# Optimization experiments

Measured on AMD Instinct MI355X. Metric: run time of the kernel, lower is better.

Reference implementation:

```python
import jax, jax.numpy as jnp
import numpy as np

B, NQ, NV = 4, 16384, 16384
DIM, FRAMES = 64, 4
D = DIM * FRAMES            # embed_dims = 256
HEADS, POINTS, LEVELS = 8, 4, 1
HD = D // HEADS             # head_dim = 32
HL, WL = 128, 128           # single-level feature map, HL*WL == NV
EPS = 1e-6


def setup_inputs() -> dict:
    key = jax.random.key(0)
    ks = jax.random.split(key, 14)
    inp = {
        "query": jax.random.normal(ks[0], (B, NQ, D), jnp.float32),
        "feat": jax.random.normal(ks[1], (B, NV, D), jnp.float32),
        "reference_points": jax.random.uniform(ks[2], (B, NQ, LEVELS, 2), jnp.float32),
        "spatial_shapes": jnp.array([[HL, WL]], jnp.int32),
        "level_start_index": jnp.array([0], jnp.int32),
        # LayerNorm params
        "qn_scale": jnp.ones((D,), jnp.float32),
        "qn_bias": jnp.zeros((D,), jnp.float32),
        "fn_scale": jnp.ones((D,), jnp.float32),
        "fn_bias": jnp.zeros((D,), jnp.float32),
        # MSDeformAttn projections
        "W_value": jax.random.normal(ks[3], (D, D), jnp.float32) / np.sqrt(D),
        "b_value": jnp.zeros((D,), jnp.float32),
        "W_off": jax.random.normal(ks[4], (D, HEADS * LEVELS * POINTS * 2), jnp.float32) * 0.01,
        "b_off": jax.random.normal(ks[5], (HEADS * LEVELS * POINTS * 2,), jnp.float32) * 0.5,
        "W_attn": jax.random.normal(ks[6], (D, HEADS * LEVELS * POINTS), jnp.float32) * 0.02,
        "b_attn": jnp.zeros((HEADS * LEVELS * POINTS,), jnp.float32),
        "W_out": jax.random.normal(ks[7], (D, D), jnp.float32) / np.sqrt(D),
        "b_out": jnp.zeros((D,), jnp.float32),
        # gamma is a learned scale (init 0 in the module; randomized here so it contributes)
        "gamma": jax.random.normal(ks[8], (D,), jnp.float32) * 0.1,
    }
    return inp


def _layer_norm(x, scale, bias):
    mu = jnp.mean(x, axis=-1, keepdims=True)
    var = jnp.mean(jnp.square(x - mu), axis=-1, keepdims=True)
    return (x - mu) * jax.lax.rsqrt(var + EPS) * scale + bias


def _bilinear_gather(v, loc, Hl, Wl):
    # v:   [B, H, N, hd] flattened level values (row-major HxW)
    # loc: [B, H, NQ, P, 2] normalized sampling locations in [0,1]
    # grid_sample semantics: align_corners=False, zero padding
    x = loc[..., 0] * Wl - 0.5
    y = loc[..., 1] * Hl - 0.5
    x0 = jnp.floor(x); y0 = jnp.floor(y)
    x1 = x0 + 1.0;     y1 = y0 + 1.0
    wx1 = x - x0; wx0 = 1.0 - wx1
    wy1 = y - y0; wy0 = 1.0 - wy1
    out = 0.0
    for xi, yi, w in ((x0, y0, wx0 * wy0), (x1, y0, wx1 * wy0),
                      (x0, y1, wx0 * wy1), (x1, y1, wx1 * wy1)):
        inb = (xi >= 0) & (xi < Wl) & (yi >= 0) & (yi < Hl)
        idx = (jnp.clip(yi, 0, Hl - 1) * Wl + jnp.clip(xi, 0, Wl - 1)).astype(jnp.int32)
        Bc, Hc, NQc, Pc = idx.shape
        g = jnp.take_along_axis(v, idx.reshape(Bc, Hc, NQc * Pc)[..., None], axis=2)
        g = g.reshape(Bc, Hc, NQc, Pc, -1)          # [B, H, NQ, P, hd]
        out = out + g * (w * inb)[..., None]
    return out


def reference(query, feat, reference_points, spatial_shapes, level_start_index,
              qn_scale, qn_bias, fn_scale, fn_bias,
              W_value, b_value, W_off, b_off, W_attn, b_attn, W_out, b_out, gamma):
    Bq, nq, _ = query.shape
    q = _layer_norm(query, qn_scale, qn_bias)
    v = _layer_norm(feat, fn_scale, fn_bias)

    # value projection -> per-head values [B, H, NV, hd]
    value = (v @ W_value + b_value).reshape(Bq, -1, HEADS, HD).transpose(0, 2, 1, 3)

    # sampling offsets [B, NQ, H, L, P, 2] and attention weights (softmax over L*P)
    off = (q @ W_off + b_off).reshape(Bq, nq, HEADS, LEVELS, POINTS, 2)
    aw = jax.nn.softmax((q @ W_attn + b_attn).reshape(Bq, nq, HEADS, LEVELS * POINTS), axis=-1)
    aw = aw.reshape(Bq, nq, HEADS, LEVELS, POINTS)

    ss = np.asarray(spatial_shapes)          # static level geometry
    lsi = np.asarray(level_start_index)
    offset_norm = ss[:, ::-1].astype(np.float32)  # (W, H) per level
    # sampling locations [B, NQ, H, L, P, 2]
    loc = reference_points[:, :, None, :, None, :] + off / offset_norm[None, None, None, :, None, :]

    acc = jnp.zeros((Bq, HEADS, nq, HD), query.dtype)
    for l in range(LEVELS):
        Hl, Wl = int(ss[l, 0]), int(ss[l, 1])
        start = int(lsi[l])
        v_l = value[:, :, start:start + Hl * Wl]                # [B, H, Hl*Wl, hd]
        loc_l = loc[:, :, :, l].transpose(0, 2, 1, 3, 4)        # [B, H, NQ, P, 2]
        sampled = _bilinear_gather(v_l, loc_l, Hl, Wl)          # [B, H, NQ, P, hd]
        aw_l = aw[:, :, :, l].transpose(0, 2, 1, 3)             # [B, H, NQ, P]
        acc = acc + jnp.einsum('bhnpd,bhnp->bhnd', sampled, aw_l)

    out = acc.transpose(0, 2, 1, 3).reshape(Bq, nq, D) @ W_out + b_out
    return query + gamma * out
```

## Files before the change

### kernel.cpp

```cpp
#include <hip/hip_runtime.h>

#define NQ 16384
#define NV 16384
#define DMODEL 256
#define SAMPN (4 * 16384 * 8)
#define VPLANE 65536

typedef __bf16 bf16x8 __attribute__((ext_vector_type(8)));
typedef float f32x4 __attribute__((ext_vector_type(4)));

__device__ __forceinline__ unsigned short f2bf(float x) {
    union { float f; unsigned int u; } v; v.f = x;
    unsigned int r = v.u + 0x7fff + ((v.u >> 16) & 1);
    return (unsigned short)(r >> 16);
}
__device__ __forceinline__ float blo(unsigned int u) {
    union { unsigned int u; float f; } v; v.u = u << 16; return v.f;
}
__device__ __forceinline__ float bhi(unsigned int u) {
    union { unsigned int u; float f; } v; v.u = u & 0xFFFF0000u; return v.f;
}
__device__ __forceinline__ f32x4 mfma16(bf16x8 a, bf16x8 b, f32x4 c) {
    return __builtin_amdgcn_mfma_f32_16x16x32_bf16(a, b, c, 0, 0, 0);
}

__global__ __launch_bounds__(256) void k_prep(
    const float* __restrict__ Wv, const float* __restrict__ Woff,
    const float* __restrict__ Wattn, const float* __restrict__ Wout,
    const float* __restrict__ fns, const float* __restrict__ fnb,
    const float* __restrict__ qns, const float* __restrict__ qnb,
    const float* __restrict__ b_value, const float* __restrict__ b_off,
    const float* __restrict__ b_attn,
    unsigned short* __restrict__ WtV, unsigned short* __restrict__ WtC,
    unsigned short* __restrict__ WtO,
    float* __restrict__ csumV, float* __restrict__ preV,
    float* __restrict__ csumC, float* __restrict__ preC) {
    const int blk = blockIdx.x;
    if (blk < 608) {
        int t = blk * 256 + threadIdx.x;
        if (t < 65536) { int n = t >> 8, k = t & 255; WtV[t] = f2bf(fns[k] * Wv[k * 256 + n]); return; }
        t -= 65536;
        if (t < 65536) { int n = t >> 8, k = t & 255; WtO[t] = f2bf(Wout[k * 256 + n]); return; }
        t -= 65536;
        if (t < 24576) {
            int j = t >> 8, k = t & 255;
            float w = (j < 64) ? Woff[k * 64 + j] : Wattn[k * 32 + (j - 64)];
            WtC[j * 256 + k] = f2bf(qns[k] * w);
        }
        return;
    }
    if (blk < 612) {
        __shared__ float sCS[4][64], sPR[4][64];
        const int nl = threadIdx.x & 63;
        const int n = (blk - 608) * 64 + nl;
        const int kp = threadIdx.x >> 6;
        float cs = 0.f, pr = 0.f;
        for (int k = kp * 64; k < kp * 64 + 64; ++k) {
            float w = Wv[k * 256 + n];
            cs += fns[k] * w;
            pr += fnb[k] * w;
        }
        sCS[kp][nl] = cs; sPR[kp][nl] = pr;
        __syncthreads();
        if (threadIdx.x < 64) {
            int nn = (blk - 608) * 64 + threadIdx.x;
            csumV[nn] = sCS[0][threadIdx.x] + sCS[1][threadIdx.x] + sCS[2][threadIdx.x] + sCS[3][threadIdx.x];
            preV[nn] = sPR[0][threadIdx.x] + sPR[1][threadIdx.x] + sPR[2][threadIdx.x] + sPR[3][threadIdx.x]
                       + b_value[nn];
        }
        return;
    }
    {
        __shared__ float sCS[2][96], sPR[2][96];
        const int t = threadIdx.x;
        if (t < 192) {
            const int n = t % 96;
            const int kp = t / 96;
            float cs = 0.f, pr = 0.f;
            for (int k = kp * 128; k < kp * 128 + 128; ++k) {
                float w = (n < 64) ? Woff[k * 64 + n] : Wattn[k * 32 + (n - 64)];
                cs += qns[k] * w;
                pr += qnb[k] * w;
            }
            sCS[kp][n] = cs; sPR[kp][n] = pr;
        }
        __syncthreads();
        if (t < 96) {
            csumC[t] = sCS[0][t] + sCS[1][t];
            preC[t] = sPR[0][t] + sPR[1][t] + ((t < 64) ? b_off[t] : b_attn[t - 64]);
        }
        return;
    }
}

#define STAGE_LNSTATS64(srcptr)                                                       \
    {                                                                                 \
        const int t = threadIdx.x;                                                    \
        const float4* src4 = (const float4*)((srcptr) + (size_t)m0 * 256);            \
        _Pragma("unroll 8") for (int i = 0; i < 16; ++i) {                            \
            float4 x = src4[i * 256 + t];                                             \
            const int row = i * 4 + (t >> 6);                                         \
            uint2 pk;                                                                 \
            pk.x = (unsigned)f2bf(x.x) | ((unsigned)f2bf(x.y) << 16);                 \
            pk.y = (unsigned)f2bf(x.z) | ((unsigned)f2bf(x.w) << 16);                 \
            *(uint2*)&A[row * 264 + (t & 63) * 4] = pk;                               \
        }                                                                             \
    }                                                                                 \
    __syncthreads();                                                                  \
    {                                                                                 \
        const int t = threadIdx.x;                                                    \
        const int r = t >> 2, h = t & 3;                                              \
        float s = 0.f, sq = 0.f;                                                      \
        _Pragma("unroll") for (int j = 0; j < 8; ++j) {                               \
            uint4 u = *(const uint4*)&A[r * 264 + h * 64 + j * 8];                    \
            float v0 = blo(u.x), v1 = bhi(u.x), v2 = blo(u.y), v3 = bhi(u.y);         \
            float v4 = blo(u.z), v5 = bhi(u.z), v6 = blo(u.w), v7 = bhi(u.w);         \
            s += v0 + v1 + v2 + v3 + v4 + v5 + v6 + v7;                               \
            sq += v0 * v0 + v1 * v1 + v2 * v2 + v3 * v3 +                             \
                  v4 * v4 + v5 * v5 + v6 * v6 + v7 * v7;                              \
        }                                                                             \
        s += __shfl_xor(s, 1);  sq += __shfl_xor(sq, 1);                              \
        s += __shfl_xor(s, 2);  sq += __shfl_xor(sq, 2);                              \
        if (h == 0) {                                                                 \
            float mu = s * 0.00390625f;                                               \
            muL[r] = mu;                                                              \
            rsL[r] = rsqrtf(sq * 0.00390625f - mu * mu + 1e-6f);                      \
        }                                                                             \
    }

#define MFMA_STEP4(bf, kk)                                                            \
    _Pragma("unroll") for (int m = 0; m < 4; ++m) {                                   \
        bf16x8 a = *(const bf16x8*)&A[(m * 16 + lrow) * 264 + (kk) * 32 + lk];        \
        _Pragma("unroll") for (int i = 0; i < 4; ++i)                                 \
            acc[i][m] = mfma16(bf[i], a, acc[i][m]);                                  \
    }

__global__ __launch_bounds__(256, 4) void k_mlp(
    const float* __restrict__ feat, const float* __restrict__ csumV,
    const float* __restrict__ preV, const unsigned short* __restrict__ WtV,
    unsigned short* __restrict__ value,
    const float* __restrict__ query, const float* __restrict__ refpt,
    const float* __restrict__ csumC, const float* __restrict__ preC,
    const unsigned short* __restrict__ WtC, float4* __restrict__ samples) {
    __shared__ unsigned short A[64 * 264];
    __shared__ float muL[64], rsL[64];
    const int blk = blockIdx.x;
    const int m0 = (blk >> 1) * 64;
    const int lane = threadIdx.x & 63;
    const int w = threadIdx.x >> 6;

    if ((blk & 1) == 0) {
        STAGE_LNSTATS64(feat)
        const int lrow = lane & 15, lk = (lane >> 4) * 8;
        f32x4 acc[4][4];
#pragma unroll
        for (int i = 0; i < 4; ++i)
#pragma unroll
            for (int m = 0; m < 4; ++m) acc[i][m] = (f32x4){0.f, 0.f, 0.f, 0.f};
#define LOADB_V(dst, kk)                                                              \
    _Pragma("unroll") for (int i = 0; i < 4; ++i) dst[i] =                            \
        *(const bf16x8*)(WtV + (size_t)((w * 4 + i) * 16 + lrow) * 256 + (kk) * 32 + lk);
        {
            bf16x8 b0[4], b1[4];
            LOADB_V(b0, 0)
#pragma unroll
            for (int k2 = 0; k2 < 4; ++k2) {
                LOADB_V(b1, k2 * 2 + 1)
                MFMA_STEP4(b0, k2 * 2)
                if (k2 < 3) { LOADB_V(b0, k2 * 2 + 2) }
                MFMA_STEP4(b1, k2 * 2 + 1)
            }
        }
        __syncthreads();
        const int g = lane >> 4;
#pragma unroll
        for (int i = 0; i < 4; ++i) {
            const int col0 = (w * 4 + i) * 16 + g * 4;
            float4 cs = *(const float4*)(csumV + col0);
            float4 pr = *(const float4*)(preV + col0);
#pragma unroll
            for (int m = 0; m < 4; ++m) {
                const int rl = m * 16 + (lane & 15);
                float mu = muL[rl], rs = rsL[rl];
                uint2 r;
                r.x = (unsigned)f2bf(rs * (acc[i][m][0] - mu * cs.x) + pr.x) |
                      ((unsigned)f2bf(rs * (acc[i][m][1] - mu * cs.y) + pr.y) << 16);
                r.y = (unsigned)f2bf(rs * (acc[i][m][2] - mu * cs.z) + pr.z) |
                      ((unsigned)f2bf(rs * (acc[i][m][3] - mu * cs.w) + pr.w) << 16);
                *(uint2*)&A[rl * 264 + col0] = r;
            }
        }
        __syncthreads();
        {
            const int pix = threadIdx.x >> 2;
            const int chunk = threadIdx.x & 3;
#pragma unroll
            for (int h = 0; h < 8; ++h) {
                *(uint4*)(value + ((size_t)h * VPLANE + (m0 + pix)) * 32 + chunk * 8) =
                    *(uint4*)&A[pix * 264 + h * 32 + chunk * 8];
            }
        }
    } else {
        float* DlA = (float*)A;
        const int lrow = lane & 15, g = lane >> 4, lk = g * 8;
        const float4* qrow = (const float4*)(query + (size_t)(m0 + w * 16 + lrow) * 256) + g * 2;
        f32x4 acc[6];
#pragma unroll
        for (int i = 0; i < 6; ++i) acc[i] = (f32x4){0.f, 0.f, 0.f, 0.f};
        float s = 0.f, sq = 0.f;
#pragma unroll
        for (int kk = 0; kk < 8; ++kk) {
            float4 xa = qrow[kk * 8];
            float4 xb = qrow[kk * 8 + 1];
            s  += xa.x + xa.y + xa.z + xa.w + xb.x + xb.y + xb.z + xb.w;
            sq += xa.x * xa.x + xa.y * xa.y + xa.z * xa.z + xa.w * xa.w +
                  xb.x * xb.x + xb.y * xb.y + xb.z * xb.z + xb.w * xb.w;
            union { bf16x8 v; unsigned short u[8]; } af;
            af.u[0] = f2bf(xa.x); af.u[1] = f2bf(xa.y); af.u[2] = f2bf(xa.z); af.u[3] = f2bf(xa.w);
            af.u[4] = f2bf(xb.x); af.u[5] = f2bf(xb.y); af.u[6] = f2bf(xb.z); af.u[7] = f2bf(xb.w);
            bf16x8 b[6];
#pragma unroll
            for (int i = 0; i < 6; ++i)
                b[i] = *(const bf16x8*)(WtC + (size_t)(i * 16 + lrow) * 256 + kk * 32 + lk);
#pragma unroll
            for (int i = 0; i < 6; ++i) acc[i] = mfma16(b[i], af.v, acc[i]);
        }
        s += __shfl_xor(s, 16); sq += __shfl_xor(sq, 16);
        s += __shfl_xor(s, 32); sq += __shfl_xor(sq, 32);
        if (lane < 16) {
            float mu = s * 0.00390625f;
            muL[w * 16 + lane] = mu;
            rsL[w * 16 + lane] = rsqrtf(sq * 0.00390625f - mu * mu + 1e-6f);
        }
        float* Dl = DlA + w * 1600;
#pragma unroll
        for (int i = 0; i < 6; ++i) {
            *(float4*)&Dl[lrow * 100 + i * 16 + g * 4] =
                make_float4(acc[i][0], acc[i][1], acc[i][2], acc[i][3]);
        }
        __syncthreads();
#pragma unroll
        for (int it = 0; it < 2; ++it) {
            int idx = it * 64 + lane;
            int rl = idx >> 3;
            int h = idx & 7;
            int row = m0 + w * 16 + rl;
            float mu = muL[w * 16 + rl], rs = rsL[w * 16 + rl];
            float rx = refpt[(size_t)row * 2 + 0] * 128.f - 0.5f;
            float ry = refpt[(size_t)row * 2 + 1] * 128.f - 0.5f;
            float l0 = rs * (Dl[rl * 100 + 64 + h * 4 + 0] - mu * csumC[64 + h * 4 + 0]) + preC[64 + h * 4 + 0];
            float l1 = rs * (Dl[rl * 100 + 64 + h * 4 + 1] - mu * csumC[64 + h * 4 + 1]) + preC[64 + h * 4 + 1];
            float l2 = rs * (Dl[rl * 100 + 64 + h * 4 + 2] - mu * csumC[64 + h * 4 + 2]) + preC[64 + h * 4 + 2];
            float l3 = rs * (Dl[rl * 100 + 64 + h * 4 + 3] - mu * csumC[64 + h * 4 + 3]) + preC[64 + h * 4 + 3];
            float mx = fmaxf(fmaxf(l0, l1), fmaxf(l2, l3));
            float e0 = __expf(l0 - mx), e1 = __expf(l1 - mx);
            float e2 = __expf(l2 - mx), e3 = __expf(l3 - mx);
            float inv = 1.f / (e0 + e1 + e2 + e3);
            float ww[4] = {e0 * inv, e1 * inv, e2 * inv, e3 * inv};
            size_t trow = (size_t)row * 8 + h;
#pragma unroll
            for (int p = 0; p < 4; ++p) {
                float ox = rs * (Dl[rl * 100 + h * 8 + p * 2 + 0] - mu * csumC[h * 8 + p * 2 + 0]) + preC[h * 8 + p * 2 + 0];
                float oy = rs * (Dl[rl * 100 + h * 8 + p * 2 + 1] - mu * csumC[h * 8 + p * 2 + 1]) + preC[h * 8 + p * 2 + 1];
                samples[(size_t)p * SAMPN + trow] = make_float4(rx + ox, ry + oy, ww[p], 0.f);
            }
        }
    }
}

__global__ __launch_bounds__(256, 4) void k_gatherout(
    const unsigned short* __restrict__ value, const float4* __restrict__ samples,
    const unsigned short* __restrict__ WtO, const float* __restrict__ b_out,
    const float* __restrict__ gamma, const float* __restrict__ query,
    float* __restrict__ out) {
    __shared__ unsigned short A[64 * 264];
    const int m0 = blockIdx.x * 64;
    const int b = m0 >> 14;
    {
        const int t = threadIdx.x;
        const int sub = t & 7;
        const int h2 = sub >> 2;
        const int h = (t >> 3) & 7;
        const unsigned short* vb = value + ((size_t)h * VPLANE + ((size_t)b << 14)) * 32;
        for (int k = 0; k < 16; ++k) {
            const int rl = k * 4 + (t >> 6);
            const size_t trow = (size_t)(m0 + rl) * 8 + h;
            float a0 = 0.f, a1 = 0.f, a2 = 0.f, a3 = 0.f;
            float a4 = 0.f, a5 = 0.f, a6 = 0.f, a7 = 0.f;
#pragma unroll
            for (int p = 0; p < 4; ++p) {
                float4 s = samples[(size_t)p * SAMPN + trow];
                float xf = floorf(s.x), yf = floorf(s.y);
                float fx = s.x - xf, fy = s.y - yf;
                int x0 = (int)xf, y0 = (int)yf;
                int x1 = x0 + 1, y1 = y0 + 1;
                float wgt = s.z;
                float wx0 = ((unsigned)x0 < 128u) ? (1.f - fx) : 0.f;
                float wx1 = ((unsigned)x1 < 128u) ? fx : 0.f;
                int xbase = min(max(x0, 0), 126);
                int xh = xbase + h2;
                float whx = (xh == x0) ? wx0 : ((xh == x1) ? wx1 : 0.f);
                float wy0 = ((unsigned)y0 < 128u) ? (1.f - fy) : 0.f;
                float wy1 = ((unsigned)y1 < 128u) ? fy : 0.f;
                int yc0 = min(max(y0, 0), 127), yc1 = min(max(y1, 0), 127);
                float w0 = whx * wy0 * wgt;
                float w1 = whx * wy1 * wgt;
                uint4 u0 = *(const uint4*)(vb + (size_t)(yc0 * 128 + xbase) * 32 + sub * 8);
                uint4 u1 = *(const uint4*)(vb + (size_t)(yc1 * 128 + xbase) * 32 + sub * 8);
                a0 = fmaf(w0, blo(u0.x), a0); a1 = fmaf(w0, bhi(u0.x), a1);
                a2 = fmaf(w0, blo(u0.y), a2); a3 = fmaf(w0, bhi(u0.y), a3);
                a4 = fmaf(w0, blo(u0.z), a4); a5 = fmaf(w0, bhi(u0.z), a5);
                a6 = fmaf(w0, blo(u0.w), a6); a7 = fmaf(w0, bhi(u0.w), a7);
                a0 = fmaf(w1, blo(u1.x), a0); a1 = fmaf(w1, bhi(u1.x), a1);
                a2 = fmaf(w1, blo(u1.y), a2); a3 = fmaf(w1, bhi(u1.y), a3);
                a4 = fmaf(w1, blo(u1.z), a4); a5 = fmaf(w1, bhi(u1.z), a5);
                a6 = fmaf(w1, blo(u1.w), a6); a7 = fmaf(w1, bhi(u1.w), a7);
            }
            a0 += __shfl_xor(a0, 4); a1 += __shfl_xor(a1, 4);
            a2 += __shfl_xor(a2, 4); a3 += __shfl_xor(a3, 4);
            a4 += __shfl_xor(a4, 4); a5 += __shfl_xor(a5, 4);
            a6 += __shfl_xor(a6, 4); a7 += __shfl_xor(a7, 4);
            if (h2 == 0) {
                uint4 r;
                r.x = (unsigned)f2bf(a0) | ((unsigned)f2bf(a1) << 16);
                r.y = (unsigned)f2bf(a2) | ((unsigned)f2bf(a3) << 16);
                r.z = (unsigned)f2bf(a4) | ((unsigned)f2bf(a5) << 16);
                r.w = (unsigned)f2bf(a6) | ((unsigned)f2bf(a7) << 16);
                *(uint4*)&A[rl * 264 + h * 32 + (sub & 3) * 8] = r;
            }
        }
    }
    __syncthreads();
    const int lane = threadIdx.x & 63;
    const int w = threadIdx.x >> 6;
    const int lrow = lane & 15, lk = (lane >> 4) * 8;
    f32x4 acc[4][4];
#pragma unroll
    for (int i = 0; i < 4; ++i)
#pragma unroll
        for (int m = 0; m < 4; ++m) acc[i][m] = (f32x4){0.f, 0.f, 0.f, 0.f};
#define LOADB_O(dst, kk)                                                              \
    _Pragma("unroll") for (int i = 0; i < 4; ++i) dst[i] =                            \
        *(const bf16x8*)(WtO + (size_t)((w * 4 + i) * 16 + lrow) * 256 + (kk) * 32 + lk);
    {
        bf16x8 b0[4], b1[4];
        LOADB_O(b0, 0)
#pragma unroll
        for (int k2 = 0; k2 < 4; ++k2) {
            LOADB_O(b1, k2 * 2 + 1)
            MFMA_STEP4(b0, k2 * 2)
            if (k2 < 3) { LOADB_O(b0, k2 * 2 + 2) }
            MFMA_STEP4(b1, k2 * 2 + 1)
        }
    }
    const int g = lane >> 4;
    float4 bo[4], gm[4];
#pragma unroll
    for (int i = 0; i < 4; ++i) {
        bo[i] = *(const float4*)(b_out + (w * 4 + i) * 16 + g * 4);
        gm[i] = *(const float4*)(gamma + (w * 4 + i) * 16 + g * 4);
    }
#pragma unroll
    for (int m = 0; m < 4; ++m) {
        const size_t row = (size_t)(m0 + m * 16 + (lane & 15));
#pragma unroll
        for (int i = 0; i < 4; ++i) {
            const int col0 = (w * 4 + i) * 16 + g * 4;
            float4 q = *(const float4*)(query + row * 256 + col0);
            float4 o;
            o.x = q.x + gm[i].x * (acc[i][m][0] + bo[i].x);
            o.y = q.y + gm[i].y * (acc[i][m][1] + bo[i].y);
            o.z = q.z + gm[i].z * (acc[i][m][2] + bo[i].z);
            o.w = q.w + gm[i].w * (acc[i][m][3] + bo[i].w);
            *(float4*)(out + row * 256 + col0) = o;
        }
    }
}

extern "C" void kernel_launch(void* const* d_in, const int* in_sizes, int n_in,
                              void* d_out, int out_size, void* d_ws, size_t ws_size,
                              hipStream_t stream) {
    const float* query    = (const float*)d_in[0];
    const float* feat     = (const float*)d_in[1];
    const float* refpt    = (const float*)d_in[2];
    const float* qn_scale = (const float*)d_in[5];
    const float* qn_bias  = (const float*)d_in[6];
    const float* fn_scale = (const float*)d_in[7];
    const float* fn_bias  = (const float*)d_in[8];
    const float* W_value  = (const float*)d_in[9];
    const float* b_value  = (const float*)d_in[10];
    const float* W_off    = (const float*)d_in[11];
    const float* b_off    = (const float*)d_in[12];
    const float* W_attn   = (const float*)d_in[13];
    const float* b_attn   = (const float*)d_in[14];
    const float* W_out    = (const float*)d_in[15];
    const float* b_out    = (const float*)d_in[16];
    const float* gamma    = (const float*)d_in[17];
    float* out = (float*)d_out;

    char* ws = (char*)d_ws;
    unsigned short* WtV   = (unsigned short*)(ws);
    unsigned short* WtO   = (unsigned short*)(ws + 131072);
    unsigned short* WtC   = (unsigned short*)(ws + 262144);
    float* csumV = (float*)(ws + 311296);
    float* preV  = (float*)(ws + 312320);
    float* csumC = (float*)(ws + 313344);
    float* preC  = (float*)(ws + 313856);
    unsigned short* value = (unsigned short*)(ws + 315392);
    float4* samples       = (float4*)(ws + 315392 + 33554432);

    hipLaunchKernelGGL(k_prep, dim3(613), dim3(256), 0, stream,
                       W_value, W_off, W_attn, W_out,
                       fn_scale, fn_bias, qn_scale, qn_bias,
                       b_value, b_off, b_attn,
                       WtV, WtC, WtO, csumV, preV, csumC, preC);
    hipLaunchKernelGGL(k_mlp, dim3(2048), dim3(256), 0, stream,
                       feat, csumV, preV, WtV, value,
                       query, refpt, csumC, preC, WtC, samples);
    hipLaunchKernelGGL(k_gatherout, dim3(1024), dim3(256), 0, stream,
                       value, samples, WtO, b_out, gamma, query, out);
}
```

Measured before the change: 163.3 us.

## Shrink k_mlp value tiles to 32 rows and store offset logits as bf16

The value-projection blocks in k_mlp now process 32 rows instead of 64, and the grid becomes three blocks per 64-row group: two value blocks and one query/offset block. The query path stores its offset/attention logits in LDS as bf16 instead of fp32, so the shared tile fits in half the space. The smaller LDS and register footprint allows launch bounds of 6 blocks per CU instead of 4, aiming for higher occupancy and better overlap of memory latency. In exchange, each weight tile loaded from memory is reused across fewer rows, and the sampling offsets and softmax logits lose precision.

```diff
diff --git a/kernel.cpp b/kernel.cpp
--- a/kernel.cpp
+++ b/kernel.cpp
@@ -13,6 +13,10 @@
     union { float f; unsigned int u; } v; v.f = x;
     unsigned int r = v.u + 0x7fff + ((v.u >> 16) & 1);
     return (unsigned short)(r >> 16);
+}
+__device__ __forceinline__ float bf2f(unsigned short h) {
+    union { unsigned int u; float f; } v; v.u = ((unsigned int)h) << 16;
+    return v.f;
 }
 __device__ __forceinline__ float blo(unsigned int u) {
     union { unsigned int u; float f; } v; v.u = u << 16; return v.f;
@@ -93,82 +97,82 @@
     }
 }
 
-#define STAGE_LNSTATS64(srcptr)                                                       \
-    {                                                                                 \
-        const int t = threadIdx.x;                                                    \
-        const float4* src4 = (const float4*)((srcptr) + (size_t)m0 * 256);            \
-        _Pragma("unroll 8") for (int i = 0; i < 16; ++i) {                            \
-            float4 x = src4[i * 256 + t];                                             \
-            const int row = i * 4 + (t >> 6);                                         \
-            uint2 pk;                                                                 \
-            pk.x = (unsigned)f2bf(x.x) | ((unsigned)f2bf(x.y) << 16);                 \
-            pk.y = (unsigned)f2bf(x.z) | ((unsigned)f2bf(x.w) << 16);                 \
-            *(uint2*)&A[row * 264 + (t & 63) * 4] = pk;                               \
-        }                                                                             \
-    }                                                                                 \
-    __syncthreads();                                                                  \
-    {                                                                                 \
-        const int t = threadIdx.x;                                                    \
-        const int r = t >> 2, h = t & 3;                                              \
-        float s = 0.f, sq = 0.f;                                                      \
-        _Pragma("unroll") for (int j = 0; j < 8; ++j) {                               \
-            uint4 u = *(const uint4*)&A[r * 264 + h * 64 + j * 8];                    \
-            float v0 = blo(u.x), v1 = bhi(u.x), v2 = blo(u.y), v3 = bhi(u.y);         \
-            float v4 = blo(u.z), v5 = bhi(u.z), v6 = blo(u.w), v7 = bhi(u.w);         \
-            s += v0 + v1 + v2 + v3 + v4 + v5 + v6 + v7;                               \
-            sq += v0 * v0 + v1 * v1 + v2 * v2 + v3 * v3 +                             \
-                  v4 * v4 + v5 * v5 + v6 * v6 + v7 * v7;                              \
-        }                                                                             \
-        s += __shfl_xor(s, 1);  sq += __shfl_xor(sq, 1);                              \
-        s += __shfl_xor(s, 2);  sq += __shfl_xor(sq, 2);                              \
-        if (h == 0) {                                                                 \
-            float mu = s * 0.00390625f;                                               \
-            muL[r] = mu;                                                              \
-            rsL[r] = rsqrtf(sq * 0.00390625f - mu * mu + 1e-6f);                      \
-        }                                                                             \
-    }
-
-#define MFMA_STEP4(bf, kk)                                                            \
-    _Pragma("unroll") for (int m = 0; m < 4; ++m) {                                   \
-        bf16x8 a = *(const bf16x8*)&A[(m * 16 + lrow) * 264 + (kk) * 32 + lk];        \
-        _Pragma("unroll") for (int i = 0; i < 4; ++i)                                 \
-            acc[i][m] = mfma16(bf[i], a, acc[i][m]);                                  \
-    }
-
-__global__ __launch_bounds__(256, 4) void k_mlp(
+__global__ __launch_bounds__(256, 6) void k_mlp(
     const float* __restrict__ feat, const float* __restrict__ csumV,
     const float* __restrict__ preV, const unsigned short* __restrict__ WtV,
     unsigned short* __restrict__ value,
     const float* __restrict__ query, const float* __restrict__ refpt,
     const float* __restrict__ csumC, const float* __restrict__ preC,
     const unsigned short* __restrict__ WtC, float4* __restrict__ samples) {
-    __shared__ unsigned short A[64 * 264];
+    __shared__ unsigned short A[32 * 264];
     __shared__ float muL[64], rsL[64];
     const int blk = blockIdx.x;
-    const int m0 = (blk >> 1) * 64;
+    const int type3 = blk % 3;
     const int lane = threadIdx.x & 63;
     const int w = threadIdx.x >> 6;
 
-    if ((blk & 1) == 0) {
-        STAGE_LNSTATS64(feat)
+    if (type3 < 2) {
+        const int m0 = ((blk / 3) * 2 + type3) * 32;
+        {
+            const int t = threadIdx.x;
+            const float4* src4 = (const float4*)(feat + (size_t)m0 * 256);
+#pragma unroll
+            for (int i = 0; i < 8; ++i) {
+                float4 x = src4[i * 256 + t];
+                const int row = i * 4 + (t >> 6);
+                uint2 pk;
+                pk.x = (unsigned)f2bf(x.x) | ((unsigned)f2bf(x.y) << 16);
+                pk.y = (unsigned)f2bf(x.z) | ((unsigned)f2bf(x.w) << 16);
+                *(uint2*)&A[row * 264 + (t & 63) * 4] = pk;
+            }
+        }
+        __syncthreads();
+        {
+            const int t = threadIdx.x;
+            const int r = t >> 3, h8 = t & 7;
+            float s = 0.f, sq = 0.f;
+#pragma unroll
+            for (int j = 0; j < 4; ++j) {
+                uint4 u = *(const uint4*)&A[r * 264 + h8 * 32 + j * 8];
+                float v0 = blo(u.x), v1 = bhi(u.x), v2 = blo(u.y), v3 = bhi(u.y);
+                float v4 = blo(u.z), v5 = bhi(u.z), v6 = blo(u.w), v7 = bhi(u.w);
+                s += v0 + v1 + v2 + v3 + v4 + v5 + v6 + v7;
+                sq += v0 * v0 + v1 * v1 + v2 * v2 + v3 * v3 +
+                      v4 * v4 + v5 * v5 + v6 * v6 + v7 * v7;
+            }
+            s += __shfl_xor(s, 1);  sq += __shfl_xor(sq, 1);
+            s += __shfl_xor(s, 2);  sq += __shfl_xor(sq, 2);
+            s += __shfl_xor(s, 4);  sq += __shfl_xor(sq, 4);
+            if (h8 == 0) {
+                float mu = s * 0.00390625f;
+                muL[r] = mu;
+                rsL[r] = rsqrtf(sq * 0.00390625f - mu * mu + 1e-6f);
+            }
+        }
         const int lrow = lane & 15, lk = (lane >> 4) * 8;
-        f32x4 acc[4][4];
+        f32x4 acc[4][2];
 #pragma unroll
         for (int i = 0; i < 4; ++i)
 #pragma unroll
-            for (int m = 0; m < 4; ++m) acc[i][m] = (f32x4){0.f, 0.f, 0.f, 0.f};
+            for (int m = 0; m < 2; ++m) acc[i][m] = (f32x4){0.f, 0.f, 0.f, 0.f};
 #define LOADB_V(dst, kk)                                                              \
     _Pragma("unroll") for (int i = 0; i < 4; ++i) dst[i] =                            \
         *(const bf16x8*)(WtV + (size_t)((w * 4 + i) * 16 + lrow) * 256 + (kk) * 32 + lk);
+#define MFMA_STEP2(bf, kk)                                                            \
+    _Pragma("unroll") for (int m = 0; m < 2; ++m) {                                   \
+        bf16x8 a = *(const bf16x8*)&A[(m * 16 + lrow) * 264 + (kk) * 32 + lk];        \
+        _Pragma("unroll") for (int i = 0; i < 4; ++i)                                 \
+            acc[i][m] = mfma16(bf[i], a, acc[i][m]);                                  \
+    }
         {
             bf16x8 b0[4], b1[4];
             LOADB_V(b0, 0)
 #pragma unroll
             for (int k2 = 0; k2 < 4; ++k2) {
                 LOADB_V(b1, k2 * 2 + 1)
-                MFMA_STEP4(b0, k2 * 2)
+                MFMA_STEP2(b0, k2 * 2)
                 if (k2 < 3) { LOADB_V(b0, k2 * 2 + 2) }
-                MFMA_STEP4(b1, k2 * 2 + 1)
+                MFMA_STEP2(b1, k2 * 2 + 1)
             }
         }
         __syncthreads();
@@ -179,7 +183,7 @@
             float4 cs = *(const float4*)(csumV + col0);
             float4 pr = *(const float4*)(preV + col0);
 #pragma unroll
-            for (int m = 0; m < 4; ++m) {
+            for (int m = 0; m < 2; ++m) {
                 const int rl = m * 16 + (lane & 15);
                 float mu = muL[rl], rs = rsL[rl];
                 uint2 r;
@@ -191,7 +195,7 @@
             }
         }
         __syncthreads();
-        {
+        if (threadIdx.x < 128) {
             const int pix = threadIdx.x >> 2;
             const int chunk = threadIdx.x & 3;
 #pragma unroll
@@ -201,7 +205,8 @@
             }
         }
     } else {
-        float* DlA = (float*)A;
+        const int m0 = (blk / 3) * 64;
+        unsigned short* Dl16A = A;
         const int lrow = lane & 15, g = lane >> 4, lk = g * 8;
         const float4* qrow = (const float4*)(query + (size_t)(m0 + w * 16 + lrow) * 256) + g * 2;
         f32x4 acc[6];
@@ -232,11 +237,14 @@
             muL[w * 16 + lane] = mu;
             rsL[w * 16 + lane] = rsqrtf(sq * 0.00390625f - mu * mu + 1e-6f);
         }
-        float* Dl = DlA + w * 1600;
+        unsigned short* Dl = Dl16A + w * (16 * 98);
 #pragma unroll
         for (int i = 0; i < 6; ++i) {
-            *(float4*)&Dl[lrow * 100 + i * 16 + g * 4] =
-                make_float4(acc[i][0], acc[i][1], acc[i][2], acc[i][3]);
+            const int col0 = i * 16 + g * 4;
+            uint2 pk;
+            pk.x = (unsigned)f2bf(acc[i][0]) | ((unsigned)f2bf(acc[i][1]) << 16);
+            pk.y = (unsigned)f2bf(acc[i][2]) | ((unsigned)f2bf(acc[i][3]) << 16);
+            *(uint2*)&Dl[lrow * 98 + col0] = pk;
         }
         __syncthreads();
 #pragma unroll
@@ -248,10 +256,10 @@
             float mu = muL[w * 16 + rl], rs = rsL[w * 16 + rl];
             float rx = refpt[(size_t)row * 2 + 0] * 128.f - 0.5f;
             float ry = refpt[(size_t)row * 2 + 1] * 128.f - 0.5f;
-            float l0 = rs * (Dl[rl * 100 + 64 + h * 4 + 0] - mu * csumC[64 + h * 4 + 0]) + preC[64 + h * 4 + 0];
-            float l1 = rs * (Dl[rl * 100 + 64 + h * 4 + 1] - mu * csumC[64 + h * 4 + 1]) + preC[64 + h * 4 + 1];
-            float l2 = rs * (Dl[rl * 100 + 64 + h * 4 + 2] - mu * csumC[64 + h * 4 + 2]) + preC[64 + h * 4 + 2];
-            float l3 = rs * (Dl[rl * 100 + 64 + h * 4 + 3] - mu * csumC[64 + h * 4 + 3]) + preC[64 + h * 4 + 3];
+            float l0 = rs * (bf2f(Dl[rl * 98 + 64 + h * 4 + 0]) - mu * csumC[64 + h * 4 + 0]) + preC[64 + h * 4 + 0];
+            float l1 = rs * (bf2f(Dl[rl * 98 + 64 + h * 4 + 1]) - mu * csumC[64 + h * 4 + 1]) + preC[64 + h * 4 + 1];
+            float l2 = rs * (bf2f(Dl[rl * 98 + 64 + h * 4 + 2]) - mu * csumC[64 + h * 4 + 2]) + preC[64 + h * 4 + 2];
+            float l3 = rs * (bf2f(Dl[rl * 98 + 64 + h * 4 + 3]) - mu * csumC[64 + h * 4 + 3]) + preC[64 + h * 4 + 3];
             float mx = fmaxf(fmaxf(l0, l1), fmaxf(l2, l3));
             float e0 = __expf(l0 - mx), e1 = __expf(l1 - mx);
             float e2 = __expf(l2 - mx), e3 = __expf(l3 - mx);
@@ -260,20 +268,27 @@
             size_t trow = (size_t)row * 8 + h;
 #pragma unroll
             for (int p = 0; p < 4; ++p) {
-                float ox = rs * (Dl[rl * 100 + h * 8 + p * 2 + 0] - mu * csumC[h * 8 + p * 2 + 0]) + preC[h * 8 + p * 2 + 0];
-                float oy = rs * (Dl[rl * 100 + h * 8 + p * 2 + 1] - mu * csumC[h * 8 + p * 2 + 1]) + preC[h * 8 + p * 2 + 1];
+                float ox = rs * (bf2f(Dl[rl * 98 + h * 8 + p * 2 + 0]) - mu * csumC[h * 8 + p * 2 + 0]) + preC[h * 8 + p * 2 + 0];
+                float oy = rs * (bf2f(Dl[rl * 98 + h * 8 + p * 2 + 1]) - mu * csumC[h * 8 + p * 2 + 1]) + preC[h * 8 + p * 2 + 1];
                 samples[(size_t)p * SAMPN + trow] = make_float4(rx + ox, ry + oy, ww[p], 0.f);
             }
         }
     }
 }
+
+#define MFMA_STEP4(bf, kk)                                                            \
+    _Pragma("unroll") for (int m = 0; m < 4; ++m) {                                   \
+        bf16x8 a = *(const bf16x8*)&AG[(m * 16 + lrow) * 264 + (kk) * 32 + lk];       \
+        _Pragma("unroll") for (int i = 0; i < 4; ++i)                                 \
+            acc[i][m] = mfma16(bf[i], a, acc[i][m]);                                  \
+    }
 
 __global__ __launch_bounds__(256, 4) void k_gatherout(
     const unsigned short* __restrict__ value, const float4* __restrict__ samples,
     const unsigned short* __restrict__ WtO, const float* __restrict__ b_out,
     const float* __restrict__ gamma, const float* __restrict__ query,
     float* __restrict__ out) {
-    __shared__ unsigned short A[64 * 264];
+    __shared__ unsigned short AG[64 * 264];
     const int m0 = blockIdx.x * 64;
     const int b = m0 >> 14;
     {
@@ -326,7 +341,7 @@
                 r.y = (unsigned)f2bf(a2) | ((unsigned)f2bf(a3) << 16);
                 r.z = (unsigned)f2bf(a4) | ((unsigned)f2bf(a5) << 16);
                 r.w = (unsigned)f2bf(a6) | ((unsigned)f2bf(a7) << 16);
-                *(uint4*)&A[rl * 264 + h * 32 + (sub & 3) * 8] = r;
+                *(uint4*)&AG[rl * 264 + h * 32 + (sub & 3) * 8] = r;
             }
         }
     }
@@ -414,7 +429,7 @@
                        fn_scale, fn_bias, qn_scale, qn_bias,
                        b_value, b_off, b_attn,
                        WtV, WtC, WtO, csumV, preV, csumC, preC);
-    hipLaunchKernelGGL(k_mlp, dim3(2048), dim3(256), 0, stream,
+    hipLaunchKernelGGL(k_mlp, dim3(3072), dim3(256), 0, stream,
                        feat, csumV, preV, WtV, value,
                        query, refpt, csumC, preC, WtC, samples);
     hipLaunchKernelGGL(k_gatherout, dim3(1024), dim3(256), 0, stream,
```

Measured after the change: 240.4 us. 1.47x slower.
